# Optimization experiments

Measured on AMD Instinct MI355X. Metric: run time of the kernel, lower is better.

## Reference

```python
import jax, jax.numpy as jnp
import numpy as np

B, S, F, E, R, O = 4, 2048, 2048, 16, 16, 2048
TEMPERATURE = 1.0


def setup_inputs() -> dict:
    key = jax.random.key(0)
    k1, k2, k3, k4 = jax.random.split(key, 4)
    x = jax.random.normal(k1, (B, S, F), dtype=jnp.float32)
    prototypes = jax.random.normal(k2, (E, F), dtype=jnp.float32)
    # prototypes are top right-singular vectors -> unit norm rows
    prototypes = prototypes / jnp.linalg.norm(prototypes, axis=1, keepdims=True)
    A_stack = jax.random.normal(k3, (E, R, F), dtype=jnp.float32) * 0.02
    B_stack = jax.random.normal(k4, (E, O, R), dtype=jnp.float32) * 0.02
    scaling = jnp.float32(2.0)
    return {"x": x, "prototypes": prototypes, "A_stack": A_stack,
            "B_stack": B_stack, "scaling": scaling, "top_k": 4}


def reference(x, prototypes, A_stack, B_stack, scaling, top_k):
    lead = x.shape[:-1]
    f_in = x.shape[-1]
    tok = x.reshape(-1, f_in)                       # (t, F)
    t = tok.shape[0]

    # Arrow routing: abs cosine-like similarity to per-expert prototypes
    sim = jnp.abs(tok @ prototypes.T)               # (t, E)
    top_v, idx = jax.lax.top_k(sim, top_k)          # (t, k)
    full_score = jnp.full(sim.shape, -jnp.inf, dtype=sim.dtype)
    full_score = full_score.at[jnp.arange(t)[:, None], idx].set(top_v)
    coeff = jax.nn.softmax(full_score / TEMPERATURE, axis=1)  # (t, E), zeros off top-k

    # Per-expert LoRA: z = tok @ A_e^T  (dense over all experts, as in source)
    z = jnp.einsum('tf,erf->ter', tok, A_stack)     # (t, E, r)
    # Combine coeff into the low-rank space before the B projection to avoid
    # materializing the (t, E, out) tensor; math identical to
    # einsum('te, teo -> to', coeff, einsum('ter,eor->teo', z, B_stack)).
    delta = jnp.einsum('te,ter,eor->to', coeff, z, B_stack)  # (t, O)

    delta = scaling * delta                          # dropout = identity (eval)
    return delta.reshape(lead + (delta.shape[-1],))
```

## Files before the change

kernel.cpp:

```cpp
#include <hip/hip_runtime.h>
#include <hip/hip_bf16.h>
#include <stdint.h>

#define T_TOKENS 8192
#define F_DIM    2048
#define E_EXP    16
#define R_RANK   16
#define O_DIM    2048
#define KDIM     (E_EXP * R_RANK)

typedef short v8s __attribute__((ext_vector_type(8)));
typedef float v4f __attribute__((ext_vector_type(4)));

#define AS1 __attribute__((address_space(1)))
#define AS3 __attribute__((address_space(3)))

__device__ __forceinline__ uint16_t f2bf(float f) {
  uint32_t u = __builtin_bit_cast(uint32_t, f);
  u += 0x7fffu + ((u >> 16) & 1u);
  return (uint16_t)(u >> 16);
}

__device__ __forceinline__ void g2lds16(const uint16_t* g, uint16_t* l) {
  __builtin_amdgcn_global_load_lds((AS1 void*)g, (AS3 void*)l, 16, 0, 0);
}

__global__ __launch_bounds__(256) void prep_weights(
    const float* __restrict__ A, const float* __restrict__ Bst,
    uint16_t* __restrict__ Ab, uint16_t* __restrict__ Bb) {
  int idx = blockIdx.x * 256 + threadIdx.x;
  if (idx < KDIM * F_DIM) {
    Ab[idx] = f2bf(A[idx]);
  }
  if (idx < O_DIM * KDIM) {
    int k = idx & (KDIM - 1);
    int o = idx >> 8;
    int e = k >> 4, r = k & 15;
    Bb[idx] = f2bf(Bst[((size_t)e * O_DIM + o) * R_RANK + r]);
  }
}

__global__ __launch_bounds__(256, 4) void route_convert(
    const float* __restrict__ x, const float* __restrict__ P,
    const float* __restrict__ scaling, const int* __restrict__ topk,
    uint16_t* __restrict__ xb, float* __restrict__ coeffS) {
  __shared__ float ps[16 * 256];

  const int tid  = threadIdx.x;
  const int lane = tid & 63;
  const int wid  = tid >> 6;
  const int t0   = blockIdx.x * 8 + wid * 2;
  const int er   = tid >> 4;
  const int eq   = tid & 15;

  float acc0[16], acc1[16];
  #pragma unroll
  for (int e = 0; e < 16; ++e) { acc0[e] = 0.f; acc1[e] = 0.f; }

  const float* xr0 = x + (size_t)t0 * F_DIM;
  const float* xr1 = x + (size_t)(t0 + 1) * F_DIM;
  uint16_t* xw0 = xb + (size_t)t0 * F_DIM;
  uint16_t* xw1 = xb + (size_t)(t0 + 1) * F_DIM;

  for (int c = 0; c < 8; ++c) {
    const int f0 = c * 256;
    __syncthreads();
    #pragma unroll
    for (int j = 0; j < 4; ++j) {
      const int col = eq * 4 + j * 64;
      *(float4*)&ps[er * 256 + col] =
          *(const float4*)&P[(size_t)er * F_DIM + f0 + col];
    }
    float4 xv0 = *(const float4*)&xr0[f0 + lane * 4];
    float4 xv1 = *(const float4*)&xr1[f0 + lane * 4];
    uint2 pk0, pk1;
    pk0.x = (uint32_t)f2bf(xv0.x) | ((uint32_t)f2bf(xv0.y) << 16);
    pk0.y = (uint32_t)f2bf(xv0.z) | ((uint32_t)f2bf(xv0.w) << 16);
    pk1.x = (uint32_t)f2bf(xv1.x) | ((uint32_t)f2bf(xv1.y) << 16);
    pk1.y = (uint32_t)f2bf(xv1.z) | ((uint32_t)f2bf(xv1.w) << 16);
    *(uint2*)&xw0[f0 + lane * 4] = pk0;
    *(uint2*)&xw1[f0 + lane * 4] = pk1;
    __syncthreads();
    #pragma unroll
    for (int e = 0; e < 16; ++e) {
      float4 pv = *(float4*)&ps[e * 256 + lane * 4];
      acc0[e] += xv0.x * pv.x; acc0[e] += xv0.y * pv.y;
      acc0[e] += xv0.z * pv.z; acc0[e] += xv0.w * pv.w;
      acc1[e] += xv1.x * pv.x; acc1[e] += xv1.y * pv.y;
      acc1[e] += xv1.z * pv.z; acc1[e] += xv1.w * pv.w;
    }
  }

  double s0[16], s1[16];
  #pragma unroll
  for (int e = 0; e < 16; ++e) {
    double d0 = (double)acc0[e];
    double d1 = (double)acc1[e];
    #pragma unroll
    for (int m = 1; m < 64; m <<= 1) {
      d0 += __shfl_xor(d0, m, 64);
      d1 += __shfl_xor(d1, m, 64);
    }
    s0[e] = fabs(d0);
    s1[e] = fabs(d1);
  }

  if (lane < 2) {
    double v[16];
    #pragma unroll
    for (int e = 0; e < 16; ++e) v[e] = lane ? s1[e] : s0[e];
    int k = topk[0];
    if (k > 16) k = 16;
    if (k < 1)  k = 1;
    unsigned mask = 0;
    double mx = 0.0;
    float ssum = 0.f;
    for (int i = 0; i < k; ++i) {
      double bv = -1.0; int bj = 0;
      #pragma unroll
      for (int j = 0; j < 16; ++j) {
        bool ok = !((mask >> j) & 1u) && (v[j] > bv);
        bv = ok ? v[j] : bv;
        bj = ok ? j  : bj;
      }
      mask |= 1u << bj;
      if (i == 0) mx = bv;
      ssum += expf((float)(bv - mx));
    }
    const float sc = scaling[0];
    float* cw = coeffS + (size_t)(t0 + lane) * 16;
    #pragma unroll
    for (int j = 0; j < 16; ++j) {
      float co = ((mask >> j) & 1u)
               ? expf((float)(v[j] - mx)) / ssum * sc : 0.f;
      cw[j] = co;
    }
  }
}

__global__ __launch_bounds__(256) void gemm_xa(
    const uint16_t* __restrict__ xb, const uint16_t* __restrict__ Ab,
    const float* __restrict__ coeffS, uint16_t* __restrict__ wb) {
  __shared__ uint16_t Xs[64 * 64];
  __shared__ uint16_t As[64 * 64];
  const int tid  = threadIdx.x;
  const int n0   = blockIdx.x * 64;
  const int m0   = blockIdx.y * 64;
  const int lane = tid & 63;
  const int wid  = tid >> 6;
  const int wm   = (wid >> 1) * 32;
  const int wn   = (wid & 1) * 32;
  const int quad = lane >> 4;
  const int cl   = lane & 15;

  const int G0 = wid * 64 + lane;
  const int G1 = G0 + 256;
  const int r0 = G0 >> 3, g0 = (G0 & 7) ^ (r0 & 7);
  const int r1 = G1 >> 3, g1 = (G1 & 7) ^ (r1 & 7);
  const uint16_t* xsrc0 = xb + (size_t)(m0 + r0) * F_DIM + g0 * 8;
  const uint16_t* xsrc1 = xb + (size_t)(m0 + r1) * F_DIM + g1 * 8;
  const uint16_t* asrc0 = Ab + (size_t)(n0 + r0) * F_DIM + g0 * 8;
  const uint16_t* asrc1 = Ab + (size_t)(n0 + r1) * F_DIM + g1 * 8;
  uint16_t* xd0 = &Xs[(wid * 64) * 8];
  uint16_t* xd1 = &Xs[(wid * 64 + 256) * 8];
  uint16_t* ad0 = &As[(wid * 64) * 8];
  uint16_t* ad1 = &As[(wid * 64 + 256) * 8];

  const int ma0 = wm + cl, ma1 = wm + 16 + cl;
  const int nb0 = wn + cl, nb1 = wn + 16 + cl;

  v4f acc[2][2];
  #pragma unroll
  for (int i = 0; i < 2; i++)
    #pragma unroll
    for (int j = 0; j < 2; j++) acc[i][j] = (v4f){0.f, 0.f, 0.f, 0.f};

  for (int k0 = 0; k0 < F_DIM; k0 += 64) {
    __syncthreads();
    g2lds16(xsrc0 + k0, xd0);
    g2lds16(xsrc1 + k0, xd1);
    g2lds16(asrc0 + k0, ad0);
    g2lds16(asrc1 + k0, ad1);
    __syncthreads();
    #pragma unroll
    for (int ks = 0; ks < 2; ++ks) {
      const int gk = ks * 4 + quad;
      v8s a0 = *(v8s*)&Xs[(ma0 * 8 + (gk ^ (ma0 & 7))) * 8];
      v8s a1 = *(v8s*)&Xs[(ma1 * 8 + (gk ^ (ma1 & 7))) * 8];
      v8s b0 = *(v8s*)&As[(nb0 * 8 + (gk ^ (nb0 & 7))) * 8];
      v8s b1 = *(v8s*)&As[(nb1 * 8 + (gk ^ (nb1 & 7))) * 8];
      acc[0][0] = __builtin_amdgcn_mfma_f32_16x16x32_bf16(a0, b0, acc[0][0], 0, 0, 0);
      acc[0][1] = __builtin_amdgcn_mfma_f32_16x16x32_bf16(a0, b1, acc[0][1], 0, 0, 0);
      acc[1][0] = __builtin_amdgcn_mfma_f32_16x16x32_bf16(a1, b0, acc[1][0], 0, 0, 0);
      acc[1][1] = __builtin_amdgcn_mfma_f32_16x16x32_bf16(a1, b1, acc[1][1], 0, 0, 0);
    }
  }

  #pragma unroll
  for (int mi = 0; mi < 2; mi++)
    #pragma unroll
    for (int ni = 0; ni < 2; ni++) {
      const int n = n0 + wn + ni * 16 + cl;
      const int eidx = n >> 4;
      #pragma unroll
      for (int reg = 0; reg < 4; reg++) {
        const int t = m0 + wm + mi * 16 + quad * 4 + reg;
        float wv = acc[mi][ni][reg] * coeffS[(size_t)t * 16 + eidx];
        wb[(size_t)t * KDIM + n] = f2bf(wv);
      }
    }
}

__global__ __launch_bounds__(256) void gemm_wb(
    const uint16_t* __restrict__ wb, const uint16_t* __restrict__ Bb,
    float* __restrict__ out) {
  __shared__ uint16_t Ws[64 * 64];
  __shared__ uint16_t Bs[64 * 64];
  const int tid  = threadIdx.x;
  const int n0   = blockIdx.x * 64;
  const int m0   = blockIdx.y * 64;
  const int lane = tid & 63;
  const int wid  = tid >> 6;
  const int wm   = (wid >> 1) * 32;
  const int wn   = (wid & 1) * 32;
  const int quad = lane >> 4;
  const int cl   = lane & 15;

  const int G0 = wid * 64 + lane;
  const int G1 = G0 + 256;
  const int r0 = G0 >> 3, g0 = (G0 & 7) ^ (r0 & 7);
  const int r1 = G1 >> 3, g1 = (G1 & 7) ^ (r1 & 7);
  const uint16_t* wsrc0 = wb + (size_t)(m0 + r0) * KDIM + g0 * 8;
  const uint16_t* wsrc1 = wb + (size_t)(m0 + r1) * KDIM + g1 * 8;
  const uint16_t* bsrc0 = Bb + (size_t)(n0 + r0) * KDIM + g0 * 8;
  const uint16_t* bsrc1 = Bb + (size_t)(n0 + r1) * KDIM + g1 * 8;
  uint16_t* wd0 = &Ws[(wid * 64) * 8];
  uint16_t* wd1 = &Ws[(wid * 64 + 256) * 8];
  uint16_t* bd0 = &Bs[(wid * 64) * 8];
  uint16_t* bd1 = &Bs[(wid * 64 + 256) * 8];

  const int ma0 = wm + cl, ma1 = wm + 16 + cl;
  const int nb0 = wn + cl, nb1 = wn + 16 + cl;

  v4f acc[2][2];
  #pragma unroll
  for (int i = 0; i < 2; i++)
    #pragma unroll
    for (int j = 0; j < 2; j++) acc[i][j] = (v4f){0.f, 0.f, 0.f, 0.f};

  for (int k0 = 0; k0 < KDIM; k0 += 64) {
    __syncthreads();
    g2lds16(wsrc0 + k0, wd0);
    g2lds16(wsrc1 + k0, wd1);
    g2lds16(bsrc0 + k0, bd0);
    g2lds16(bsrc1 + k0, bd1);
    __syncthreads();
    #pragma unroll
    for (int ks = 0; ks < 2; ++ks) {
      const int gk = ks * 4 + quad;
      v8s a0 = *(v8s*)&Ws[(ma0 * 8 + (gk ^ (ma0 & 7))) * 8];
      v8s a1 = *(v8s*)&Ws[(ma1 * 8 + (gk ^ (ma1 & 7))) * 8];
      v8s b0 = *(v8s*)&Bs[(nb0 * 8 + (gk ^ (nb0 & 7))) * 8];
      v8s b1 = *(v8s*)&Bs[(nb1 * 8 + (gk ^ (nb1 & 7))) * 8];
      acc[0][0] = __builtin_amdgcn_mfma_f32_16x16x32_bf16(a0, b0, acc[0][0], 0, 0, 0);
      acc[0][1] = __builtin_amdgcn_mfma_f32_16x16x32_bf16(a0, b1, acc[0][1], 0, 0, 0);
      acc[1][0] = __builtin_amdgcn_mfma_f32_16x16x32_bf16(a1, b0, acc[1][0], 0, 0, 0);
      acc[1][1] = __builtin_amdgcn_mfma_f32_16x16x32_bf16(a1, b1, acc[1][1], 0, 0, 0);
    }
  }

  #pragma unroll
  for (int mi = 0; mi < 2; mi++)
    #pragma unroll
    for (int ni = 0; ni < 2; ni++) {
      const int o = n0 + wn + ni * 16 + cl;
      #pragma unroll
      for (int reg = 0; reg < 4; reg++) {
        const int t = m0 + wm + mi * 16 + quad * 4 + reg;
        out[(size_t)t * O_DIM + o] = acc[mi][ni][reg];
      }
    }
}

extern "C" void kernel_launch(void* const* d_in, const int* in_sizes, int n_in,
                              void* d_out, int out_size, void* d_ws, size_t ws_size,
                              hipStream_t stream) {
  (void)in_sizes; (void)n_in; (void)out_size; (void)ws_size;
  const float* x       = (const float*)d_in[0];
  const float* P       = (const float*)d_in[1];
  const float* A       = (const float*)d_in[2];
  const float* Bst     = (const float*)d_in[3];
  const float* scaling = (const float*)d_in[4];
  const int*   topk    = (const int*)d_in[5];
  float* out = (float*)d_out;

  char* ws = (char*)d_ws;
  uint16_t* xb     = (uint16_t*)(ws);
  uint16_t* Ab     = (uint16_t*)(ws + 33554432);
  uint16_t* Bb     = (uint16_t*)(ws + 34603008);
  uint16_t* wbuf   = (uint16_t*)(ws + 35651584);
  float*    coeffS = (float*)   (ws + 39845888);

  hipLaunchKernelGGL(prep_weights, dim3(2048), dim3(256), 0, stream, A, Bst, Ab, Bb);
  hipLaunchKernelGGL(route_convert, dim3(T_TOKENS / 8), dim3(256), 0, stream,
                     x, P, scaling, topk, xb, coeffS);
  hipLaunchKernelGGL(gemm_xa, dim3(KDIM / 64, T_TOKENS / 64), dim3(256), 0, stream,
                     xb, Ab, coeffS, wbuf);
  hipLaunchKernelGGL(gemm_wb, dim3(O_DIM / 64, T_TOKENS / 64), dim3(256), 0, stream,
                     wbuf, Bb, out);
}
```

Baseline: 203.4 us.

## Split routing into streaming partial-sum and top-k kernels; stage GEMM epilogues in LDS

Routing is split in two. A streaming kernel now runs on a 2D grid over feature chunks and token groups: it converts x to bf16 and writes per-chunk similarity partials. A separate per-token kernel sums those partials in double precision and does the top-k softmax. This replaces the old kernel's double-precision 64-lane shuffle reductions and its repeated prototype reloads. Both GEMMs now load two 64-wide K slices per barrier pair, which halves the number of synchronizations. Their epilogues go through shared memory so each thread writes a full 16-byte vector instead of scattered narrow stores. The cost is an extra kernel launch plus a 4 MB partials round-trip, which reuses the wbuf workspace region.

```diff
diff --git a/kernel.cpp b/kernel.cpp
--- a/kernel.cpp
+++ b/kernel.cpp
@@ -40,109 +40,158 @@
   }
 }
 
-__global__ __launch_bounds__(256, 4) void route_convert(
+__global__ __launch_bounds__(256) void route_stream(
     const float* __restrict__ x, const float* __restrict__ P,
-    const float* __restrict__ scaling, const int* __restrict__ topk,
-    uint16_t* __restrict__ xb, float* __restrict__ coeffS) {
-  __shared__ float ps[16 * 256];
-
-  const int tid  = threadIdx.x;
-  const int lane = tid & 63;
-  const int wid  = tid >> 6;
-  const int t0   = blockIdx.x * 8 + wid * 2;
-  const int er   = tid >> 4;
-  const int eq   = tid & 15;
-
-  float acc0[16], acc1[16];
-  #pragma unroll
-  for (int e = 0; e < 16; ++e) { acc0[e] = 0.f; acc1[e] = 0.f; }
-
-  const float* xr0 = x + (size_t)t0 * F_DIM;
-  const float* xr1 = x + (size_t)(t0 + 1) * F_DIM;
-  uint16_t* xw0 = xb + (size_t)t0 * F_DIM;
-  uint16_t* xw1 = xb + (size_t)(t0 + 1) * F_DIM;
-
+    uint16_t* __restrict__ xb, float4* __restrict__ partials4) {
+  __shared__ float ps[16 * 260];
+  const int tid = threadIdx.x;
+  const int c   = blockIdx.x;
+  const int by  = blockIdx.y;
+  const int f0  = c * 256;
+
+  {
+    const int e = tid >> 4;
+    #pragma unroll
+    for (int j = 0; j < 4; ++j) {
+      const int col = (tid & 15) * 4 + j * 64;
+      *(float4*)&ps[e * 260 + col] =
+          *(const float4*)&P[(size_t)e * F_DIM + f0 + col];
+    }
+  }
+  __syncthreads();
+
+  const int sub = tid & 15;
+  const int tg  = tid >> 4;
+  const int t0  = by * 64 + tg * 4;
+  const float* xr = x + (size_t)t0 * F_DIM + f0;
+  uint16_t*    xw = xb + (size_t)t0 * F_DIM + f0;
+
+  float a0[16], a1[16], a2[16], a3[16];
+  #pragma unroll
+  for (int e = 0; e < 16; ++e) { a0[e] = 0.f; a1[e] = 0.f; a2[e] = 0.f; a3[e] = 0.f; }
+
+  #pragma unroll
+  for (int j = 0; j < 4; ++j) {
+    const int off = sub * 4 + j * 64;
+    float4 v0 = *(const float4*)&xr[off];
+    float4 v1 = *(const float4*)&xr[F_DIM + off];
+    float4 v2 = *(const float4*)&xr[2 * F_DIM + off];
+    float4 v3 = *(const float4*)&xr[3 * F_DIM + off];
+    uint2 p0, p1, p2, p3;
+    p0.x = (uint32_t)f2bf(v0.x) | ((uint32_t)f2bf(v0.y) << 16);
+    p0.y = (uint32_t)f2bf(v0.z) | ((uint32_t)f2bf(v0.w) << 16);
+    p1.x = (uint32_t)f2bf(v1.x) | ((uint32_t)f2bf(v1.y) << 16);
+    p1.y = (uint32_t)f2bf(v1.z) | ((uint32_t)f2bf(v1.w) << 16);
+    p2.x = (uint32_t)f2bf(v2.x) | ((uint32_t)f2bf(v2.y) << 16);
+    p2.y = (uint32_t)f2bf(v2.z) | ((uint32_t)f2bf(v2.w) << 16);
+    p3.x = (uint32_t)f2bf(v3.x) | ((uint32_t)f2bf(v3.y) << 16);
+    p3.y = (uint32_t)f2bf(v3.z) | ((uint32_t)f2bf(v3.w) << 16);
+    *(uint2*)&xw[off]             = p0;
+    *(uint2*)&xw[F_DIM + off]     = p1;
+    *(uint2*)&xw[2 * F_DIM + off] = p2;
+    *(uint2*)&xw[3 * F_DIM + off] = p3;
+    #pragma unroll
+    for (int e = 0; e < 16; ++e) {
+      float4 pv = *(float4*)&ps[e * 260 + off];
+      a0[e] += v0.x * pv.x; a0[e] += v0.y * pv.y; a0[e] += v0.z * pv.z; a0[e] += v0.w * pv.w;
+      a1[e] += v1.x * pv.x; a1[e] += v1.y * pv.y; a1[e] += v1.z * pv.z; a1[e] += v1.w * pv.w;
+      a2[e] += v2.x * pv.x; a2[e] += v2.y * pv.y; a2[e] += v2.z * pv.z; a2[e] += v2.w * pv.w;
+      a3[e] += v3.x * pv.x; a3[e] += v3.y * pv.y; a3[e] += v3.z * pv.z; a3[e] += v3.w * pv.w;
+    }
+  }
+
+  #pragma unroll
+  for (int e = 0; e < 16; ++e) {
+    #pragma unroll
+    for (int m = 1; m < 16; m <<= 1) {
+      a0[e] += __shfl_xor(a0[e], m, 64);
+      a1[e] += __shfl_xor(a1[e], m, 64);
+      a2[e] += __shfl_xor(a2[e], m, 64);
+      a3[e] += __shfl_xor(a3[e], m, 64);
+    }
+  }
+
+  const size_t cb = (size_t)c * 4;
+  if (sub == 0) {
+    #pragma unroll
+    for (int e4 = 0; e4 < 4; ++e4)
+      partials4[(cb + e4) * T_TOKENS + t0] =
+          make_float4(a0[e4 * 4], a0[e4 * 4 + 1], a0[e4 * 4 + 2], a0[e4 * 4 + 3]);
+  } else if (sub == 1) {
+    #pragma unroll
+    for (int e4 = 0; e4 < 4; ++e4)
+      partials4[(cb + e4) * T_TOKENS + t0 + 1] =
+          make_float4(a1[e4 * 4], a1[e4 * 4 + 1], a1[e4 * 4 + 2], a1[e4 * 4 + 3]);
+  } else if (sub == 2) {
+    #pragma unroll
+    for (int e4 = 0; e4 < 4; ++e4)
+      partials4[(cb + e4) * T_TOKENS + t0 + 2] =
+          make_float4(a2[e4 * 4], a2[e4 * 4 + 1], a2[e4 * 4 + 2], a2[e4 * 4 + 3]);
+  } else if (sub == 3) {
+    #pragma unroll
+    for (int e4 = 0; e4 < 4; ++e4)
+      partials4[(cb + e4) * T_TOKENS + t0 + 3] =
+          make_float4(a3[e4 * 4], a3[e4 * 4 + 1], a3[e4 * 4 + 2], a3[e4 * 4 + 3]);
+  }
+}
+
+__global__ __launch_bounds__(256) void route_topk(
+    const float4* __restrict__ partials4, const float* __restrict__ scaling,
+    const int* __restrict__ topk, float* __restrict__ coeffS) {
+  const int t = blockIdx.x * 256 + threadIdx.x;
+  double s[16];
+  #pragma unroll
+  for (int e = 0; e < 16; ++e) s[e] = 0.0;
   for (int c = 0; c < 8; ++c) {
-    const int f0 = c * 256;
-    __syncthreads();
-    #pragma unroll
-    for (int j = 0; j < 4; ++j) {
-      const int col = eq * 4 + j * 64;
-      *(float4*)&ps[er * 256 + col] =
-          *(const float4*)&P[(size_t)er * F_DIM + f0 + col];
-    }
-    float4 xv0 = *(const float4*)&xr0[f0 + lane * 4];
-    float4 xv1 = *(const float4*)&xr1[f0 + lane * 4];
-    uint2 pk0, pk1;
-    pk0.x = (uint32_t)f2bf(xv0.x) | ((uint32_t)f2bf(xv0.y) << 16);
-    pk0.y = (uint32_t)f2bf(xv0.z) | ((uint32_t)f2bf(xv0.w) << 16);
-    pk1.x = (uint32_t)f2bf(xv1.x) | ((uint32_t)f2bf(xv1.y) << 16);
-    pk1.y = (uint32_t)f2bf(xv1.z) | ((uint32_t)f2bf(xv1.w) << 16);
-    *(uint2*)&xw0[f0 + lane * 4] = pk0;
-    *(uint2*)&xw1[f0 + lane * 4] = pk1;
-    __syncthreads();
-    #pragma unroll
-    for (int e = 0; e < 16; ++e) {
-      float4 pv = *(float4*)&ps[e * 256 + lane * 4];
-      acc0[e] += xv0.x * pv.x; acc0[e] += xv0.y * pv.y;
-      acc0[e] += xv0.z * pv.z; acc0[e] += xv0.w * pv.w;
-      acc1[e] += xv1.x * pv.x; acc1[e] += xv1.y * pv.y;
-      acc1[e] += xv1.z * pv.z; acc1[e] += xv1.w * pv.w;
-    }
-  }
-
-  double s0[16], s1[16];
-  #pragma unroll
-  for (int e = 0; e < 16; ++e) {
-    double d0 = (double)acc0[e];
-    double d1 = (double)acc1[e];
-    #pragma unroll
-    for (int m = 1; m < 64; m <<= 1) {
-      d0 += __shfl_xor(d0, m, 64);
-      d1 += __shfl_xor(d1, m, 64);
-    }
-    s0[e] = fabs(d0);
-    s1[e] = fabs(d1);
-  }
-
-  if (lane < 2) {
-    double v[16];
-    #pragma unroll
-    for (int e = 0; e < 16; ++e) v[e] = lane ? s1[e] : s0[e];
-    int k = topk[0];
-    if (k > 16) k = 16;
-    if (k < 1)  k = 1;
-    unsigned mask = 0;
-    double mx = 0.0;
-    float ssum = 0.f;
-    for (int i = 0; i < k; ++i) {
-      double bv = -1.0; int bj = 0;
-      #pragma unroll
-      for (int j = 0; j < 16; ++j) {
-        bool ok = !((mask >> j) & 1u) && (v[j] > bv);
-        bv = ok ? v[j] : bv;
-        bj = ok ? j  : bj;
-      }
-      mask |= 1u << bj;
-      if (i == 0) mx = bv;
-      ssum += expf((float)(bv - mx));
-    }
-    const float sc = scaling[0];
-    float* cw = coeffS + (size_t)(t0 + lane) * 16;
+    #pragma unroll
+    for (int e4 = 0; e4 < 4; ++e4) {
+      float4 p = partials4[((size_t)c * 4 + e4) * T_TOKENS + t];
+      s[e4 * 4]     += (double)p.x;
+      s[e4 * 4 + 1] += (double)p.y;
+      s[e4 * 4 + 2] += (double)p.z;
+      s[e4 * 4 + 3] += (double)p.w;
+    }
+  }
+  double v[16];
+  #pragma unroll
+  for (int e = 0; e < 16; ++e) v[e] = fabs(s[e]);
+
+  int k = topk[0];
+  if (k > 16) k = 16;
+  if (k < 1)  k = 1;
+  unsigned mask = 0;
+  double mx = 0.0;
+  float ssum = 0.f;
+  for (int i = 0; i < k; ++i) {
+    double bv = -1.0; int bj = 0;
     #pragma unroll
     for (int j = 0; j < 16; ++j) {
-      float co = ((mask >> j) & 1u)
-               ? expf((float)(v[j] - mx)) / ssum * sc : 0.f;
-      cw[j] = co;
-    }
-  }
+      bool ok = !((mask >> j) & 1u) && (v[j] > bv);
+      bv = ok ? v[j] : bv;
+      bj = ok ? j  : bj;
+    }
+    mask |= 1u << bj;
+    if (i == 0) mx = bv;
+    ssum += expf((float)(bv - mx));
+  }
+  const float sc = scaling[0];
+  float co[16];
+  #pragma unroll
+  for (int j = 0; j < 16; ++j)
+    co[j] = ((mask >> j) & 1u) ? expf((float)(v[j] - mx)) / ssum * sc : 0.f;
+  float* cw = coeffS + (size_t)t * 16;
+  #pragma unroll
+  for (int j4 = 0; j4 < 4; ++j4)
+    *(float4*)&cw[j4 * 4] = make_float4(co[j4 * 4], co[j4 * 4 + 1],
+                                        co[j4 * 4 + 2], co[j4 * 4 + 3]);
 }
 
 __global__ __launch_bounds__(256) void gemm_xa(
     const uint16_t* __restrict__ xb, const uint16_t* __restrict__ Ab,
     const float* __restrict__ coeffS, uint16_t* __restrict__ wb) {
-  __shared__ uint16_t Xs[64 * 64];
-  __shared__ uint16_t As[64 * 64];
+  __shared__ uint16_t S[16384];
+  uint16_t* Xh[2] = { S,         S + 4096  };
+  uint16_t* Ah[2] = { S + 8192,  S + 12288 };
   const int tid  = threadIdx.x;
   const int n0   = blockIdx.x * 64;
   const int m0   = blockIdx.y * 64;
@@ -157,14 +206,12 @@
   const int G1 = G0 + 256;
   const int r0 = G0 >> 3, g0 = (G0 & 7) ^ (r0 & 7);
   const int r1 = G1 >> 3, g1 = (G1 & 7) ^ (r1 & 7);
-  const uint16_t* xsrc0 = xb + (size_t)(m0 + r0) * F_DIM + g0 * 8;
-  const uint16_t* xsrc1 = xb + (size_t)(m0 + r1) * F_DIM + g1 * 8;
-  const uint16_t* asrc0 = Ab + (size_t)(n0 + r0) * F_DIM + g0 * 8;
-  const uint16_t* asrc1 = Ab + (size_t)(n0 + r1) * F_DIM + g1 * 8;
-  uint16_t* xd0 = &Xs[(wid * 64) * 8];
-  uint16_t* xd1 = &Xs[(wid * 64 + 256) * 8];
-  uint16_t* ad0 = &As[(wid * 64) * 8];
-  uint16_t* ad1 = &As[(wid * 64 + 256) * 8];
+  const uint16_t* xs0 = xb + (size_t)(m0 + r0) * F_DIM + g0 * 8;
+  const uint16_t* xs1 = xb + (size_t)(m0 + r1) * F_DIM + g1 * 8;
+  const uint16_t* as0 = Ab + (size_t)(n0 + r0) * F_DIM + g0 * 8;
+  const uint16_t* as1 = Ab + (size_t)(n0 + r1) * F_DIM + g1 * 8;
+  const int d0 = wid * 512;
+  const int d1 = wid * 512 + 2048;
 
   const int ma0 = wm + cl, ma1 = wm + 16 + cl;
   const int nb0 = wn + cl, nb1 = wn + 16 + cl;
@@ -175,47 +222,65 @@
     #pragma unroll
     for (int j = 0; j < 2; j++) acc[i][j] = (v4f){0.f, 0.f, 0.f, 0.f};
 
-  for (int k0 = 0; k0 < F_DIM; k0 += 64) {
+  for (int k0 = 0; k0 < F_DIM; k0 += 128) {
     __syncthreads();
-    g2lds16(xsrc0 + k0, xd0);
-    g2lds16(xsrc1 + k0, xd1);
-    g2lds16(asrc0 + k0, ad0);
-    g2lds16(asrc1 + k0, ad1);
+    g2lds16(xs0 + k0,      Xh[0] + d0);
+    g2lds16(xs1 + k0,      Xh[0] + d1);
+    g2lds16(as0 + k0,      Ah[0] + d0);
+    g2lds16(as1 + k0,      Ah[0] + d1);
+    g2lds16(xs0 + k0 + 64, Xh[1] + d0);
+    g2lds16(xs1 + k0 + 64, Xh[1] + d1);
+    g2lds16(as0 + k0 + 64, Ah[1] + d0);
+    g2lds16(as1 + k0 + 64, Ah[1] + d1);
     __syncthreads();
     #pragma unroll
-    for (int ks = 0; ks < 2; ++ks) {
-      const int gk = ks * 4 + quad;
-      v8s a0 = *(v8s*)&Xs[(ma0 * 8 + (gk ^ (ma0 & 7))) * 8];
-      v8s a1 = *(v8s*)&Xs[(ma1 * 8 + (gk ^ (ma1 & 7))) * 8];
-      v8s b0 = *(v8s*)&As[(nb0 * 8 + (gk ^ (nb0 & 7))) * 8];
-      v8s b1 = *(v8s*)&As[(nb1 * 8 + (gk ^ (nb1 & 7))) * 8];
-      acc[0][0] = __builtin_amdgcn_mfma_f32_16x16x32_bf16(a0, b0, acc[0][0], 0, 0, 0);
-      acc[0][1] = __builtin_amdgcn_mfma_f32_16x16x32_bf16(a0, b1, acc[0][1], 0, 0, 0);
-      acc[1][0] = __builtin_amdgcn_mfma_f32_16x16x32_bf16(a1, b0, acc[1][0], 0, 0, 0);
-      acc[1][1] = __builtin_amdgcn_mfma_f32_16x16x32_bf16(a1, b1, acc[1][1], 0, 0, 0);
-    }
-  }
-
+    for (int h = 0; h < 2; ++h) {
+      #pragma unroll
+      for (int ks = 0; ks < 2; ++ks) {
+        const int gk = ks * 4 + quad;
+        v8s fa0 = *(v8s*)&Xh[h][(ma0 * 8 + (gk ^ (ma0 & 7))) * 8];
+        v8s fa1 = *(v8s*)&Xh[h][(ma1 * 8 + (gk ^ (ma1 & 7))) * 8];
+        v8s fb0 = *(v8s*)&Ah[h][(nb0 * 8 + (gk ^ (nb0 & 7))) * 8];
+        v8s fb1 = *(v8s*)&Ah[h][(nb1 * 8 + (gk ^ (nb1 & 7))) * 8];
+        acc[0][0] = __builtin_amdgcn_mfma_f32_16x16x32_bf16(fa0, fb0, acc[0][0], 0, 0, 0);
+        acc[0][1] = __builtin_amdgcn_mfma_f32_16x16x32_bf16(fa0, fb1, acc[0][1], 0, 0, 0);
+        acc[1][0] = __builtin_amdgcn_mfma_f32_16x16x32_bf16(fa1, fb0, acc[1][0], 0, 0, 0);
+        acc[1][1] = __builtin_amdgcn_mfma_f32_16x16x32_bf16(fa1, fb1, acc[1][1], 0, 0, 0);
+      }
+    }
+  }
+
+  __syncthreads();
+  uint16_t* tile = S;
   #pragma unroll
   for (int mi = 0; mi < 2; mi++)
     #pragma unroll
     for (int ni = 0; ni < 2; ni++) {
-      const int n = n0 + wn + ni * 16 + cl;
-      const int eidx = n >> 4;
+      const int nl = wn + ni * 16 + cl;
+      const int eidx = (n0 + nl) >> 4;
       #pragma unroll
       for (int reg = 0; reg < 4; reg++) {
-        const int t = m0 + wm + mi * 16 + quad * 4 + reg;
-        float wv = acc[mi][ni][reg] * coeffS[(size_t)t * 16 + eidx];
-        wb[(size_t)t * KDIM + n] = f2bf(wv);
+        const int tl = wm + mi * 16 + quad * 4 + reg;
+        float wv = acc[mi][ni][reg] * coeffS[(size_t)(m0 + tl) * 16 + eidx];
+        tile[tl * 72 + nl] = f2bf(wv);
       }
     }
+  __syncthreads();
+  #pragma unroll
+  for (int p = 0; p < 2; ++p) {
+    const int row  = p * 32 + (tid >> 3);
+    const int colg = (tid & 7) * 8;
+    uint4 val = *(uint4*)&tile[row * 72 + colg];
+    *(uint4*)&wb[(size_t)(m0 + row) * KDIM + n0 + colg] = val;
+  }
 }
 
 __global__ __launch_bounds__(256) void gemm_wb(
     const uint16_t* __restrict__ wb, const uint16_t* __restrict__ Bb,
     float* __restrict__ out) {
-  __shared__ uint16_t Ws[64 * 64];
-  __shared__ uint16_t Bs[64 * 64];
+  __shared__ uint16_t S[16384];
+  uint16_t* Wh[2] = { S,         S + 4096  };
+  uint16_t* Bh[2] = { S + 8192,  S + 12288 };
   const int tid  = threadIdx.x;
   const int n0   = blockIdx.x * 64;
   const int m0   = blockIdx.y * 64;
@@ -230,14 +295,12 @@
   const int G1 = G0 + 256;
   const int r0 = G0 >> 3, g0 = (G0 & 7) ^ (r0 & 7);
   const int r1 = G1 >> 3, g1 = (G1 & 7) ^ (r1 & 7);
-  const uint16_t* wsrc0 = wb + (size_t)(m0 + r0) * KDIM + g0 * 8;
-  const uint16_t* wsrc1 = wb + (size_t)(m0 + r1) * KDIM + g1 * 8;
-  const uint16_t* bsrc0 = Bb + (size_t)(n0 + r0) * KDIM + g0 * 8;
-  const uint16_t* bsrc1 = Bb + (size_t)(n0 + r1) * KDIM + g1 * 8;
-  uint16_t* wd0 = &Ws[(wid * 64) * 8];
-  uint16_t* wd1 = &Ws[(wid * 64 + 256) * 8];
-  uint16_t* bd0 = &Bs[(wid * 64) * 8];
-  uint16_t* bd1 = &Bs[(wid * 64 + 256) * 8];
+  const uint16_t* ws0 = wb + (size_t)(m0 + r0) * KDIM + g0 * 8;
+  const uint16_t* ws1 = wb + (size_t)(m0 + r1) * KDIM + g1 * 8;
+  const uint16_t* bs0 = Bb + (size_t)(n0 + r0) * KDIM + g0 * 8;
+  const uint16_t* bs1 = Bb + (size_t)(n0 + r1) * KDIM + g1 * 8;
+  const int d0 = wid * 512;
+  const int d1 = wid * 512 + 2048;
 
   const int ma0 = wm + cl, ma1 = wm + 16 + cl;
   const int nb0 = wn + cl, nb1 = wn + 16 + cl;
@@ -248,38 +311,56 @@
     #pragma unroll
     for (int j = 0; j < 2; j++) acc[i][j] = (v4f){0.f, 0.f, 0.f, 0.f};
 
-  for (int k0 = 0; k0 < KDIM; k0 += 64) {
+  #pragma unroll
+  for (int k0 = 0; k0 < KDIM; k0 += 128) {
     __syncthreads();
-    g2lds16(wsrc0 + k0, wd0);
-    g2lds16(wsrc1 + k0, wd1);
-    g2lds16(bsrc0 + k0, bd0);
-    g2lds16(bsrc1 + k0, bd1);
+    g2lds16(ws0 + k0,      Wh[0] + d0);
+    g2lds16(ws1 + k0,      Wh[0] + d1);
+    g2lds16(bs0 + k0,      Bh[0] + d0);
+    g2lds16(bs1 + k0,      Bh[0] + d1);
+    g2lds16(ws0 + k0 + 64, Wh[1] + d0);
+    g2lds16(ws1 + k0 + 64, Wh[1] + d1);
+    g2lds16(bs0 + k0 + 64, Bh[1] + d0);
+    g2lds16(bs1 + k0 + 64, Bh[1] + d1);
     __syncthreads();
     #pragma unroll
-    for (int ks = 0; ks < 2; ++ks) {
-      const int gk = ks * 4 + quad;
-      v8s a0 = *(v8s*)&Ws[(ma0 * 8 + (gk ^ (ma0 & 7))) * 8];
-      v8s a1 = *(v8s*)&Ws[(ma1 * 8 + (gk ^ (ma1 & 7))) * 8];
-      v8s b0 = *(v8s*)&Bs[(nb0 * 8 + (gk ^ (nb0 & 7))) * 8];
-      v8s b1 = *(v8s*)&Bs[(nb1 * 8 + (gk ^ (nb1 & 7))) * 8];
-      acc[0][0] = __builtin_amdgcn_mfma_f32_16x16x32_bf16(a0, b0, acc[0][0], 0, 0, 0);
-      acc[0][1] = __builtin_amdgcn_mfma_f32_16x16x32_bf16(a0, b1, acc[0][1], 0, 0, 0);
-      acc[1][0] = __builtin_amdgcn_mfma_f32_16x16x32_bf16(a1, b0, acc[1][0], 0, 0, 0);
-      acc[1][1] = __builtin_amdgcn_mfma_f32_16x16x32_bf16(a1, b1, acc[1][1], 0, 0, 0);
-    }
-  }
-
+    for (int h = 0; h < 2; ++h) {
+      #pragma unroll
+      for (int ks = 0; ks < 2; ++ks) {
+        const int gk = ks * 4 + quad;
+        v8s fa0 = *(v8s*)&Wh[h][(ma0 * 8 + (gk ^ (ma0 & 7))) * 8];
+        v8s fa1 = *(v8s*)&Wh[h][(ma1 * 8 + (gk ^ (ma1 & 7))) * 8];
+        v8s fb0 = *(v8s*)&Bh[h][(nb0 * 8 + (gk ^ (nb0 & 7))) * 8];
+        v8s fb1 = *(v8s*)&Bh[h][(nb1 * 8 + (gk ^ (nb1 & 7))) * 8];
+        acc[0][0] = __builtin_amdgcn_mfma_f32_16x16x32_bf16(fa0, fb0, acc[0][0], 0, 0, 0);
+        acc[0][1] = __builtin_amdgcn_mfma_f32_16x16x32_bf16(fa0, fb1, acc[0][1], 0, 0, 0);
+        acc[1][0] = __builtin_amdgcn_mfma_f32_16x16x32_bf16(fa1, fb0, acc[1][0], 0, 0, 0);
+        acc[1][1] = __builtin_amdgcn_mfma_f32_16x16x32_bf16(fa1, fb1, acc[1][1], 0, 0, 0);
+      }
+    }
+  }
+
+  __syncthreads();
+  float* ft = (float*)S;
   #pragma unroll
   for (int mi = 0; mi < 2; mi++)
     #pragma unroll
     for (int ni = 0; ni < 2; ni++) {
-      const int o = n0 + wn + ni * 16 + cl;
+      const int nl = wn + ni * 16 + cl;
       #pragma unroll
       for (int reg = 0; reg < 4; reg++) {
-        const int t = m0 + wm + mi * 16 + quad * 4 + reg;
-        out[(size_t)t * O_DIM + o] = acc[mi][ni][reg];
+        const int tl = wm + mi * 16 + quad * 4 + reg;
+        ft[tl * 68 + nl] = acc[mi][ni][reg];
       }
     }
+  __syncthreads();
+  #pragma unroll
+  for (int p = 0; p < 4; ++p) {
+    const int row = p * 16 + (tid >> 4);
+    const int col = (tid & 15) * 4;
+    float4 val = *(float4*)&ft[row * 68 + col];
+    *(float4*)&out[(size_t)(m0 + row) * O_DIM + n0 + col] = val;
+  }
 }
 
 extern "C" void kernel_launch(void* const* d_in, const int* in_sizes, int n_in,
@@ -298,12 +379,14 @@
   uint16_t* xb     = (uint16_t*)(ws);
   uint16_t* Ab     = (uint16_t*)(ws + 33554432);
   uint16_t* Bb     = (uint16_t*)(ws + 34603008);
+  float4*   parts  = (float4*)  (ws + 35651584);
   uint16_t* wbuf   = (uint16_t*)(ws + 35651584);
   float*    coeffS = (float*)   (ws + 39845888);
 
   hipLaunchKernelGGL(prep_weights, dim3(2048), dim3(256), 0, stream, A, Bst, Ab, Bb);
-  hipLaunchKernelGGL(route_convert, dim3(T_TOKENS / 8), dim3(256), 0, stream,
-                     x, P, scaling, topk, xb, coeffS);
+  hipLaunchKernelGGL(route_stream, dim3(8, 128), dim3(256), 0, stream, x, P, xb, parts);
+  hipLaunchKernelGGL(route_topk, dim3(T_TOKENS / 256), dim3(256), 0, stream,
+                     parts, scaling, topk, coeffS);
   hipLaunchKernelGGL(gemm_xa, dim3(KDIM / 64, T_TOKENS / 64), dim3(256), 0, stream,
                      xb, Ab, coeffS, wbuf);
   hipLaunchKernelGGL(gemm_wb, dim3(O_DIM / 64, T_TOKENS / 64), dim3(256), 0, stream,
```

New measurement: 189.3 us. 1.07x faster.
